# Kernel optimization log

Hardware: AMD Instinct MI355X
Metric: run time of the kernel (lower is better)

Reference implementation:

```python
import jax, jax.numpy as jnp
import numpy as np

B, E, M, H, NH = 256, 16384, 65536, 128, 4
HD = H // NH
LQ, LK = 128, 384  # padded lengths for to_dense_batch (safe upper bounds on group size)


def to_dense_batch(x, batch, num_graphs, max_len):
    # batch is sorted; position within group = global index - group start
    n = x.shape[0]
    start = jnp.searchsorted(batch, jnp.arange(num_graphs))
    pos = jnp.clip(jnp.arange(n) - start[batch], 0, max_len - 1)
    dense = jnp.zeros((num_graphs, max_len, x.shape[-1]), x.dtype).at[batch, pos].set(x)
    mask = jnp.zeros((num_graphs, max_len), bool).at[batch, pos].set(True)
    return dense, mask, pos


def setup_inputs() -> dict:
    key = jax.random.key(0)
    ks = jax.random.split(key, 9)
    edge_attr = jax.random.normal(ks[0], (E, H), jnp.float32)
    edge_index = jax.random.randint(ks[1], (2, E), 0, 4096)
    incoming_edges_list = jax.random.randint(ks[2], (M,), 0, E)
    incoming_edges_batch = jnp.sort(jax.random.randint(ks[3], (M,), 0, B))
    edge_batch = jnp.sort(jax.random.randint(ks[4], (E,), 0, B))
    s = 1.0 / np.sqrt(H)
    s2 = 1.0 / np.sqrt(2 * H)
    in_proj_w = jax.random.uniform(ks[5], (3 * H, H), jnp.float32, -s, s)
    in_proj_b = jnp.zeros((3 * H,), jnp.float32)
    out_proj_w = jax.random.uniform(ks[6], (H, H), jnp.float32, -s, s)
    out_proj_b = jnp.zeros((H,), jnp.float32)
    w1 = jax.random.uniform(ks[7], (2 * H, H), jnp.float32, -s, s)
    b1 = jnp.zeros((2 * H,), jnp.float32)
    w2 = jax.random.uniform(ks[8], (H, 2 * H), jnp.float32, -s2, s2)
    b2 = jnp.zeros((H,), jnp.float32)
    return dict(edge_index=edge_index, edge_attr=edge_attr,
                incoming_edges_list=incoming_edges_list,
                incoming_edges_batch=incoming_edges_batch, edge_batch=edge_batch,
                in_proj_w=in_proj_w, in_proj_b=in_proj_b,
                out_proj_w=out_proj_w, out_proj_b=out_proj_b,
                w1=w1, b1=b1, w2=w2, b2=b2)


def reference(edge_index, edge_attr, incoming_edges_list, incoming_edges_batch,
              edge_batch, in_proj_w, in_proj_b, out_proj_w, out_proj_b,
              w1, b1, w2, b2):
    # pad queries (edges per graph) and keys (gathered incoming messages per graph)
    q_dense, q_mask, q_pos = to_dense_batch(edge_attr, edge_batch, B, LQ)
    gathered = edge_attr[incoming_edges_list]                     # [M, H]
    k_dense, k_mask, _ = to_dense_batch(gathered, incoming_edges_batch, B, LK)

    wq, wk, wv = in_proj_w[:H], in_proj_w[H:2 * H], in_proj_w[2 * H:]
    bq, bk, bv = in_proj_b[:H], in_proj_b[H:2 * H], in_proj_b[2 * H:]
    q = (q_dense @ wq.T + bq).reshape(B, LQ, NH, HD)
    k = (k_dense @ wk.T + bk).reshape(B, LK, NH, HD)
    v = (k_dense @ wv.T + bv).reshape(B, LK, NH, HD)

    logits = jnp.einsum('bqhd,bkhd->bhqk', q, k) / np.sqrt(HD)
    logits = jnp.where(k_mask[:, None, None, :], logits, -1e9)   # key_padding_mask
    attn = jax.nn.softmax(logits, axis=-1)
    ctx = jnp.einsum('bhqk,bkhd->bqhd', attn, v).reshape(B, LQ, H)
    att_dense = ctx @ out_proj_w.T + out_proj_b                   # [B, LQ, H]

    # scatter back to ragged edge order (equiv. to dense[mask] for sorted batch)
    updated = att_dense[edge_batch, q_pos]                        # [E, H]
    att = edge_attr + updated
    ffn = jax.nn.relu(att @ w1.T + b1) @ w2.T + b2
    return att + ffn
```

## Files before the change

### kernel.cpp

```cpp
#include <hip/hip_runtime.h>
#include <hip/hip_bf16.h>

constexpr int B  = 256;
constexpr int E  = 16384;
constexpr int M  = 65536;
constexpr int H  = 128;
constexpr int NH = 4;
constexpr int HD = 32;
constexpr int LQ = 128;
constexpr int LK = 384;

constexpr int WQ_OFF  = 0;
constexpr int WK_OFF  = 16384;
constexpr int WV_OFF  = 32768;
constexpr int OPW_OFF = 49152;
constexpr int W1_OFF  = 65536;
constexpr int W2_OFF  = 98304;
constexpr int W_TOTAL = 131072;

typedef __attribute__((ext_vector_type(8))) short bf16x8;
typedef __attribute__((ext_vector_type(8))) unsigned short u16x8;
typedef __attribute__((ext_vector_type(4))) float f32x4;

__device__ __forceinline__ ushort f2bf(float x) {
  union { float f; unsigned u; } v; v.f = x;
  unsigned r = (v.u + 0x7FFFu + ((v.u >> 16) & 1u)) >> 16;
  return (ushort)r;
}
__device__ __forceinline__ unsigned pack2bf(float a, float b) {
  return (unsigned)f2bf(a) | ((unsigned)f2bf(b) << 16);
}

__global__ __launch_bounds__(256) void k_starts_prep(
    const int* __restrict__ eb, const int* __restrict__ ieb,
    int* __restrict__ sq, int* __restrict__ sk,
    const float* __restrict__ in_proj_w, const float* __restrict__ opw,
    const float* __restrict__ w1, const float* __restrict__ w2,
    ushort* __restrict__ Wb) {
  const int bx = blockIdx.x, t = threadIdx.x;
  if (bx == 0) {
    for (int i = t; i <= B; i += 256) {
      int lo = 0, hi = E;
      while (lo < hi) { int mid = (lo + hi) >> 1; if (eb[mid] < i) lo = mid + 1; else hi = mid; }
      sq[i] = lo;
      lo = 0; hi = M;
      while (lo < hi) { int mid = (lo + hi) >> 1; if (ieb[mid] < i) lo = mid + 1; else hi = mid; }
      sk[i] = lo;
    }
  } else {
    int i = ((bx - 1) * 256 + t) * 4;
    if (i < W_TOTAL) {
      float4 v;
      if (i < OPW_OFF)      v = *(const float4*)(in_proj_w + i);
      else if (i < W1_OFF)  v = *(const float4*)(opw + (i - OPW_OFF));
      else if (i < W2_OFF)  v = *(const float4*)(w1 + (i - W1_OFF));
      else                  v = *(const float4*)(w2 + (i - W2_OFF));
      ushort4 o; o.x = f2bf(v.x); o.y = f2bf(v.y); o.z = f2bf(v.z); o.w = f2bf(v.w);
      *(ushort4*)(Wb + i) = o;
    }
  }
}

__global__ __launch_bounds__(256) void k_proj_all(
    const float* __restrict__ edge_attr, const ushort* __restrict__ Wb,
    const float* __restrict__ in_proj_b,
    ushort* __restrict__ Qall, ushort* __restrict__ Kall, ushort* __restrict__ Vall) {
  constexpr int IP = 136;
  __shared__ ushort inL[32 * IP];
  const int t = threadIdx.x;
  const int row0 = blockIdx.x * 32;
  for (int idx = t; idx < 32 * 32; idx += 256) {
    int r = idx >> 5, c = idx & 31;
    float4 v = ((const float4*)(edge_attr + (size_t)(row0 + r) * H))[c];
    ushort4 o; o.x = f2bf(v.x); o.y = f2bf(v.y); o.z = f2bf(v.z); o.w = f2bf(v.w);
    *(ushort4*)(inL + r * IP + c * 4) = o;
  }
  __syncthreads();
  const int w = t >> 6, lane = t & 63, g = lane >> 4, l15 = lane & 15;
  const int wr = (w & 1) * 16, ch = w >> 1;
  bf16x8 a[4];
#pragma unroll
  for (int kc = 0; kc < 4; kc++)
    a[kc] = *(const bf16x8*)(inL + (wr + l15) * IP + kc * 32 + g * 8);
  const int row = row0 + wr + l15;
#pragma unroll
  for (int p = 0; p < 3; p++) {
    const int woff = WQ_OFF + p * 16384;
    const float* bias = in_proj_b + p * H;
    ushort* dst = (p == 0) ? Qall : (p == 1) ? Kall : Vall;
#pragma unroll
    for (int ci = 0; ci < 4; ci++) {
      int ct = ch * 4 + ci;
      f32x4 acc = {0.f, 0.f, 0.f, 0.f};
#pragma unroll
      for (int kc = 0; kc < 4; kc++) {
        bf16x8 bw = *(const bf16x8*)(Wb + woff + (size_t)(ct * 16 + l15) * H + kc * 32 + g * 8);
        acc = __builtin_amdgcn_mfma_f32_16x16x32_bf16(bw, a[kc], acc, 0, 0, 0);
      }
      int oc = ct * 16 + 4 * g;
      float4 bb = *(const float4*)(bias + oc);
      ushort4 v;
      v.x = f2bf(acc[0] + bb.x); v.y = f2bf(acc[1] + bb.y);
      v.z = f2bf(acc[2] + bb.z); v.w = f2bf(acc[3] + bb.w);
      *(ushort4*)(dst + (size_t)row * H + oc) = v;
    }
  }
}

__global__ __launch_bounds__(256, 4) void k_attn_g(
    const ushort* __restrict__ Qall, const ushort* __restrict__ Kall,
    const ushort* __restrict__ Vall, const int* __restrict__ iel,
    const float* __restrict__ in_proj_b,
    const int* __restrict__ sq, const int* __restrict__ sk,
    ushort* __restrict__ CtxB) {
  constexpr int VP = 388;
  __shared__ ushort VTl[HD * VP];
  __shared__ int srcL[LK];

  const int b = blockIdx.x, h = blockIdx.y;
  const int t = threadIdx.x;
  const int q0 = sq[b], lenq = sq[b + 1] - q0;
  const int k0 = sk[b], lenk = sk[b + 1] - k0;
  const int nq = lenq < LQ ? lenq : LQ;
  const int nk = lenk < LK ? lenk : LK;
  const int nkc = (nk + 63) & ~63;
  const int nqt = (nq + 15) >> 4;

  const int w = t >> 6, lane = t & 63, g = lane >> 4, l15 = lane & 15;
  const int chb = h * HD;

  for (int idx = t; idx < nk; idx += 256) {
    int kj = k0 + idx;
    if (lenk > LK && idx == LK - 1) kj = k0 + lenk - 1;
    srcL[idx] = iel[kj];
  }
  for (int idx = t; idx < nk * 4; idx += 256) {
    int row = idx >> 2, c = idx & 3;
    int kj = k0 + row;
    if (lenk > LK && row == LK - 1) kj = k0 + lenk - 1;
    int src = iel[kj];
    u16x8 v = *(const u16x8*)(Vall + (size_t)src * H + chb + c * 8);
#pragma unroll
    for (int j = 0; j < 8; j++) VTl[(c * 8 + j) * VP + row] = v[j];
  }
  for (int idx = t; idx < ((nkc - nk) << 5); idx += 256) {
    int d = idx & 31, k = nk + (idx >> 5);
    VTl[d * VP + k] = 0;
  }
  __syncthreads();

  const float scale = 0.17677669529663687f;
  for (int qt = w; qt < nqt; qt += 4) {
    int slot = qt * 16 + l15;
    bool valid = slot < nq;
    int src = q0 + slot;
    if (lenq > LQ && slot == LQ - 1) src = q0 + lenq - 1;
    if (!valid) src = q0;
    bf16x8 bq = *(const bf16x8*)(Qall + (size_t)src * H + chb + g * 8);

    f32x4 o0 = {0.f, 0.f, 0.f, 0.f}, o1 = {0.f, 0.f, 0.f, 0.f};
    float m = -3.0e38f, s = 0.f;
    for (int kc = 0; kc < nk; kc += 64) {
      int r0 = kc + l15, r1 = kc + 16 + l15, r2 = kc + 32 + l15, r3 = kc + 48 + l15;
      int s0_ = (r0 < nk) ? srcL[r0] : 0;
      int s1_ = (r1 < nk) ? srcL[r1] : 0;
      int s2_ = (r2 < nk) ? srcL[r2] : 0;
      int s3_ = (r3 < nk) ? srcL[r3] : 0;
      bf16x8 a0 = *(const bf16x8*)(Kall + (size_t)s0_ * H + chb + g * 8);
      bf16x8 a1 = *(const bf16x8*)(Kall + (size_t)s1_ * H + chb + g * 8);
      bf16x8 a2 = *(const bf16x8*)(Kall + (size_t)s2_ * H + chb + g * 8);
      bf16x8 a3 = *(const bf16x8*)(Kall + (size_t)s3_ * H + chb + g * 8);
      f32x4 z = {0.f, 0.f, 0.f, 0.f};
      f32x4 st0 = __builtin_amdgcn_mfma_f32_16x16x32_bf16(a0, bq, z, 0, 0, 0);
      f32x4 st1 = __builtin_amdgcn_mfma_f32_16x16x32_bf16(a1, bq, z, 0, 0, 0);
      f32x4 st2 = __builtin_amdgcn_mfma_f32_16x16x32_bf16(a2, bq, z, 0, 0, 0);
      f32x4 st3 = __builtin_amdgcn_mfma_f32_16x16x32_bf16(a3, bq, z, 0, 0, 0);
      float p[16];
#pragma unroll
      for (int r = 0; r < 4; r++) {
        p[r]      = (kc + 4 * g + r < nk)      ? st0[r] * scale : -1e30f;
        p[4 + r]  = (kc + 16 + 4 * g + r < nk) ? st1[r] * scale : -1e30f;
        p[8 + r]  = (kc + 32 + 4 * g + r < nk) ? st2[r] * scale : -1e30f;
        p[12 + r] = (kc + 48 + 4 * g + r < nk) ? st3[r] * scale : -1e30f;
      }
      float pm = p[0];
#pragma unroll
      for (int r = 1; r < 16; r++) pm = fmaxf(pm, p[r]);
      pm = fmaxf(pm, __shfl_xor(pm, 16));
      pm = fmaxf(pm, __shfl_xor(pm, 32));
      float mn = fmaxf(m, pm);
      float corr = __expf(m - mn);
      float rs = 0.f;
#pragma unroll
      for (int r = 0; r < 16; r++) { p[r] = __expf(p[r] - mn); rs += p[r]; }
      rs += __shfl_xor(rs, 16);
      rs += __shfl_xor(rs, 32);
      s = s * corr + rs;
      m = mn;
      unsigned pkw[4][2];
#pragma unroll
      for (int i = 0; i < 4; i++) {
        pkw[i][0] = pack2bf(p[4 * i + 0], p[4 * i + 1]);
        pkw[i][1] = pack2bf(p[4 * i + 2], p[4 * i + 3]);
      }
      union { int i[4]; bf16x8 v; } pb0, pb1;
#pragma unroll
      for (int j = 0; j < 4; j++) {
        int sl = (2 * (g & 1) + (j >> 1)) * 16 + l15;
        int a_ = __shfl((int)pkw[0][j & 1], sl);
        int b_ = __shfl((int)pkw[1][j & 1], sl);
        int c_ = __shfl((int)pkw[2][j & 1], sl);
        int d_ = __shfl((int)pkw[3][j & 1], sl);
        pb0.i[j] = (g < 2) ? a_ : b_;
        pb1.i[j] = (g < 2) ? c_ : d_;
      }
      bf16x8 av00 = *(const bf16x8*)(VTl + l15 * VP + kc + 8 * g);
      bf16x8 av01 = *(const bf16x8*)(VTl + l15 * VP + kc + 32 + 8 * g);
      bf16x8 av10 = *(const bf16x8*)(VTl + (16 + l15) * VP + kc + 8 * g);
      bf16x8 av11 = *(const bf16x8*)(VTl + (16 + l15) * VP + kc + 32 + 8 * g);
#pragma unroll
      for (int r = 0; r < 4; r++) { o0[r] *= corr; o1[r] *= corr; }
      o0 = __builtin_amdgcn_mfma_f32_16x16x32_bf16(av00, pb0.v, o0, 0, 0, 0);
      o0 = __builtin_amdgcn_mfma_f32_16x16x32_bf16(av01, pb1.v, o0, 0, 0, 0);
      o1 = __builtin_amdgcn_mfma_f32_16x16x32_bf16(av10, pb0.v, o1, 0, 0, 0);
      o1 = __builtin_amdgcn_mfma_f32_16x16x32_bf16(av11, pb1.v, o1, 0, 0, 0);
    }
    if (valid) {
      int qi = q0 + slot;
      if (lenq > LQ && slot == LQ - 1) qi = q0 + lenq - 1;
      ushort* outp = CtxB + (size_t)qi * H + chb;
      if (nk > 0) {
        float inv = 1.f / s;
        ushort4 v0, v1;
#pragma unroll
        for (int r = 0; r < 4; r++) { ((ushort*)&v0)[r] = f2bf(o0[r] * inv); ((ushort*)&v1)[r] = f2bf(o1[r] * inv); }
        *(ushort4*)(outp + 4 * g) = v0;
        *(ushort4*)(outp + 16 + 4 * g) = v1;
      } else {
        const float* bv = in_proj_b + 2 * H + chb;
        ushort4 v0, v1;
#pragma unroll
        for (int r = 0; r < 4; r++) { ((ushort*)&v0)[r] = f2bf(bv[4 * g + r]); ((ushort*)&v1)[r] = f2bf(bv[16 + 4 * g + r]); }
        *(ushort4*)(outp + 4 * g) = v0;
        *(ushort4*)(outp + 16 + 4 * g) = v1;
      }
    }
  }
}

__global__ __launch_bounds__(256) void k_out_ffn_mfma(
    const ushort* __restrict__ CtxB, const float* __restrict__ edge_attr,
    const int* __restrict__ sq, const int* __restrict__ eb,
    const ushort* __restrict__ Wb, const float* __restrict__ opb,
    const float* __restrict__ b1, const float* __restrict__ b2,
    float* __restrict__ out) {
  constexpr int IP = 136;
  constexpr int HP = 264;
  __shared__ ushort attB[16 * IP];
  __shared__ ushort h1L[16 * HP];
  const int t = threadIdx.x;
  const int row0 = blockIdx.x * 16;

  for (int idx = t; idx < 16 * 16; idx += 256) {
    int r = idx >> 4, c = idx & 15;
    int i = row0 + r;
    int bb = eb[i];
    int qq0 = sq[bb];
    int lenq = sq[bb + 1] - qq0;
    int src = i;
    if (lenq > LQ && (i - qq0) >= LQ - 1) src = qq0 + lenq - 1;
    *(u16x8*)(attB + r * IP + c * 8) = *(const u16x8*)(CtxB + (size_t)src * H + c * 8);
  }
  __syncthreads();

  const int w = t >> 6, lane = t & 63, g = lane >> 4, l15 = lane & 15;
  const int row = row0 + l15;
  bf16x8 ca[4];
#pragma unroll
  for (int kc = 0; kc < 4; kc++)
    ca[kc] = *(const bf16x8*)(attB + l15 * IP + kc * 32 + g * 8);
  __syncthreads();

  float att[2][4];
#pragma unroll
  for (int ci = 0; ci < 2; ci++) {
    int ct = w * 2 + ci;
    f32x4 acc = {0.f, 0.f, 0.f, 0.f};
#pragma unroll
    for (int kc = 0; kc < 4; kc++) {
      bf16x8 bw = *(const bf16x8*)(Wb + OPW_OFF + (size_t)(ct * 16 + l15) * H + kc * 32 + g * 8);
      acc = __builtin_amdgcn_mfma_f32_16x16x32_bf16(bw, ca[kc], acc, 0, 0, 0);
    }
    int oc = ct * 16 + 4 * g;
    float4 bo = *(const float4*)(opb + oc);
    float4 ea = *(const float4*)(edge_attr + (size_t)row * H + oc);
    ushort4 v;
    att[ci][0] = acc[0] + bo.x + ea.x; v.x = f2bf(att[ci][0]);
    att[ci][1] = acc[1] + bo.y + ea.y; v.y = f2bf(att[ci][1]);
    att[ci][2] = acc[2] + bo.z + ea.z; v.z = f2bf(att[ci][2]);
    att[ci][3] = acc[3] + bo.w + ea.w; v.w = f2bf(att[ci][3]);
    *(ushort4*)(attB + l15 * IP + oc) = v;
  }
  __syncthreads();

  bf16x8 aa[4];
#pragma unroll
  for (int kc = 0; kc < 4; kc++)
    aa[kc] = *(const bf16x8*)(attB + l15 * IP + kc * 32 + g * 8);
#pragma unroll
  for (int ci = 0; ci < 4; ci++) {
    int ct = w * 4 + ci;
    f32x4 acc = {0.f, 0.f, 0.f, 0.f};
#pragma unroll
    for (int kc = 0; kc < 4; kc++) {
      bf16x8 bw = *(const bf16x8*)(Wb + W1_OFF + (size_t)(ct * 16 + l15) * H + kc * 32 + g * 8);
      acc = __builtin_amdgcn_mfma_f32_16x16x32_bf16(bw, aa[kc], acc, 0, 0, 0);
    }
    int oc = ct * 16 + 4 * g;
    float4 bb = *(const float4*)(b1 + oc);
    ushort4 v;
    v.x = f2bf(fmaxf(acc[0] + bb.x, 0.f)); v.y = f2bf(fmaxf(acc[1] + bb.y, 0.f));
    v.z = f2bf(fmaxf(acc[2] + bb.z, 0.f)); v.w = f2bf(fmaxf(acc[3] + bb.w, 0.f));
    *(ushort4*)(h1L + l15 * HP + oc) = v;
  }
  __syncthreads();

  bf16x8 ha[8];
#pragma unroll
  for (int kc = 0; kc < 8; kc++)
    ha[kc] = *(const bf16x8*)(h1L + l15 * HP + kc * 32 + g * 8);
#pragma unroll
  for (int ci = 0; ci < 2; ci++) {
    int ct = w * 2 + ci;
    f32x4 acc = {0.f, 0.f, 0.f, 0.f};
#pragma unroll
    for (int kc = 0; kc < 8; kc++) {
      bf16x8 bw = *(const bf16x8*)(Wb + W2_OFF + (size_t)(ct * 16 + l15) * 2 * H + kc * 32 + g * 8);
      acc = __builtin_amdgcn_mfma_f32_16x16x32_bf16(bw, ha[kc], acc, 0, 0, 0);
    }
    int oc = ct * 16 + 4 * g;
    float4 bb = *(const float4*)(b2 + oc);
    float4 o;
    o.x = att[ci][0] + acc[0] + bb.x;
    o.y = att[ci][1] + acc[1] + bb.y;
    o.z = att[ci][2] + acc[2] + bb.z;
    o.w = att[ci][3] + acc[3] + bb.w;
    *(float4*)(out + (size_t)row * H + oc) = o;
  }
}

extern "C" void kernel_launch(void* const* d_in, const int* in_sizes, int n_in,
                              void* d_out, int out_size, void* d_ws, size_t ws_size,
                              hipStream_t stream) {
  const float* edge_attr = (const float*)d_in[1];
  const int*   iel       = (const int*)d_in[2];
  const int*   ieb       = (const int*)d_in[3];
  const int*   eb        = (const int*)d_in[4];
  const float* in_proj_w = (const float*)d_in[5];
  const float* in_proj_b = (const float*)d_in[6];
  const float* opw       = (const float*)d_in[7];
  const float* opb       = (const float*)d_in[8];
  const float* w1        = (const float*)d_in[9];
  const float* b1        = (const float*)d_in[10];
  const float* w2        = (const float*)d_in[11];
  const float* b2        = (const float*)d_in[12];
  float* out = (float*)d_out;

  char* ws = (char*)d_ws;
  int* sq = (int*)ws;
  int* sk = (int*)(ws + 2048);
  ushort* CtxB = (ushort*)(ws + 4096);
  ushort* Wb   = CtxB + (size_t)E * H;
  ushort* Qall = Wb + W_TOTAL;
  ushort* Kall = Qall + (size_t)E * H;
  ushort* Vall = Kall + (size_t)E * H;

  k_starts_prep<<<dim3(129), dim3(256), 0, stream>>>(eb, ieb, sq, sk, in_proj_w, opw, w1, w2, Wb);
  k_proj_all<<<dim3(E / 32), dim3(256), 0, stream>>>(edge_attr, Wb, in_proj_b, Qall, Kall, Vall);
  k_attn_g<<<dim3(B, NH), dim3(256), 0, stream>>>(Qall, Kall, Vall, iel, in_proj_b, sq, sk, CtxB);
  k_out_ffn_mfma<<<dim3(E / 16), dim3(256), 0, stream>>>(CtxB, edge_attr, sq, eb, Wb, opb, b1, b2, out);
}
```

Baseline: 83.30 us.

## Drop prep kernel, convert weights inline, and store Q/K/V head-major

Removes the separate prep kernel. Group starts are now found by binary search inside the attention and FFN kernels, and fp32 weights are converted to bf16 on load inside the MFMA loops. Q/K/V are stored head-major ([NH][E][HD]), so each gathered 64-byte row is contiguous per head, and V gathers reuse the shared srcL indices. This saves one launch and its serialization, at the cost of reading fp32 weights twice as wide and repeating the conversion in every block.

```diff
diff --git a/kernel.cpp b/kernel.cpp
--- a/kernel.cpp
+++ b/kernel.cpp
@@ -10,14 +10,6 @@
 constexpr int LQ = 128;
 constexpr int LK = 384;
 
-constexpr int WQ_OFF  = 0;
-constexpr int WK_OFF  = 16384;
-constexpr int WV_OFF  = 32768;
-constexpr int OPW_OFF = 49152;
-constexpr int W1_OFF  = 65536;
-constexpr int W2_OFF  = 98304;
-constexpr int W_TOTAL = 131072;
-
 typedef __attribute__((ext_vector_type(8))) short bf16x8;
 typedef __attribute__((ext_vector_type(8))) unsigned short u16x8;
 typedef __attribute__((ext_vector_type(4))) float f32x4;
@@ -30,41 +22,21 @@
 __device__ __forceinline__ unsigned pack2bf(float a, float b) {
   return (unsigned)f2bf(a) | ((unsigned)f2bf(b) << 16);
 }
-
-__global__ __launch_bounds__(256) void k_starts_prep(
-    const int* __restrict__ eb, const int* __restrict__ ieb,
-    int* __restrict__ sq, int* __restrict__ sk,
-    const float* __restrict__ in_proj_w, const float* __restrict__ opw,
-    const float* __restrict__ w1, const float* __restrict__ w2,
-    ushort* __restrict__ Wb) {
-  const int bx = blockIdx.x, t = threadIdx.x;
-  if (bx == 0) {
-    for (int i = t; i <= B; i += 256) {
-      int lo = 0, hi = E;
-      while (lo < hi) { int mid = (lo + hi) >> 1; if (eb[mid] < i) lo = mid + 1; else hi = mid; }
-      sq[i] = lo;
-      lo = 0; hi = M;
-      while (lo < hi) { int mid = (lo + hi) >> 1; if (ieb[mid] < i) lo = mid + 1; else hi = mid; }
-      sk[i] = lo;
-    }
-  } else {
-    int i = ((bx - 1) * 256 + t) * 4;
-    if (i < W_TOTAL) {
-      float4 v;
-      if (i < OPW_OFF)      v = *(const float4*)(in_proj_w + i);
-      else if (i < W1_OFF)  v = *(const float4*)(opw + (i - OPW_OFF));
-      else if (i < W2_OFF)  v = *(const float4*)(w1 + (i - W1_OFF));
-      else                  v = *(const float4*)(w2 + (i - W2_OFF));
-      ushort4 o; o.x = f2bf(v.x); o.y = f2bf(v.y); o.z = f2bf(v.z); o.w = f2bf(v.w);
-      *(ushort4*)(Wb + i) = o;
-    }
-  }
+__device__ __forceinline__ bf16x8 ldw8(const float* __restrict__ p) {
+  float4 a = *(const float4*)p;
+  float4 b = *(const float4*)(p + 4);
+  union { unsigned u[4]; bf16x8 v; } r;
+  r.u[0] = pack2bf(a.x, a.y);
+  r.u[1] = pack2bf(a.z, a.w);
+  r.u[2] = pack2bf(b.x, b.y);
+  r.u[3] = pack2bf(b.z, b.w);
+  return r.v;
 }
 
 __global__ __launch_bounds__(256) void k_proj_all(
-    const float* __restrict__ edge_attr, const ushort* __restrict__ Wb,
+    const float* __restrict__ edge_attr, const float* __restrict__ in_proj_w,
     const float* __restrict__ in_proj_b,
-    ushort* __restrict__ Qall, ushort* __restrict__ Kall, ushort* __restrict__ Vall) {
+    ushort* __restrict__ Qh, ushort* __restrict__ Kh, ushort* __restrict__ Vh) {
   constexpr int IP = 136;
   __shared__ ushort inL[32 * IP];
   const int t = threadIdx.x;
@@ -85,16 +57,15 @@
   const int row = row0 + wr + l15;
 #pragma unroll
   for (int p = 0; p < 3; p++) {
-    const int woff = WQ_OFF + p * 16384;
     const float* bias = in_proj_b + p * H;
-    ushort* dst = (p == 0) ? Qall : (p == 1) ? Kall : Vall;
+    ushort* dst = (p == 0) ? Qh : (p == 1) ? Kh : Vh;
 #pragma unroll
     for (int ci = 0; ci < 4; ci++) {
       int ct = ch * 4 + ci;
       f32x4 acc = {0.f, 0.f, 0.f, 0.f};
 #pragma unroll
       for (int kc = 0; kc < 4; kc++) {
-        bf16x8 bw = *(const bf16x8*)(Wb + woff + (size_t)(ct * 16 + l15) * H + kc * 32 + g * 8);
+        bf16x8 bw = ldw8(in_proj_w + (size_t)(p * H + ct * 16 + l15) * H + kc * 32 + g * 8);
         acc = __builtin_amdgcn_mfma_f32_16x16x32_bf16(bw, a[kc], acc, 0, 0, 0);
       }
       int oc = ct * 16 + 4 * g;
@@ -102,31 +73,43 @@
       ushort4 v;
       v.x = f2bf(acc[0] + bb.x); v.y = f2bf(acc[1] + bb.y);
       v.z = f2bf(acc[2] + bb.z); v.w = f2bf(acc[3] + bb.w);
-      *(ushort4*)(dst + (size_t)row * H + oc) = v;
+      *(ushort4*)(dst + (size_t)(oc >> 5) * E * HD + (size_t)row * HD + (oc & 31)) = v;
     }
   }
 }
 
 __global__ __launch_bounds__(256, 4) void k_attn_g(
-    const ushort* __restrict__ Qall, const ushort* __restrict__ Kall,
-    const ushort* __restrict__ Vall, const int* __restrict__ iel,
-    const float* __restrict__ in_proj_b,
-    const int* __restrict__ sq, const int* __restrict__ sk,
-    ushort* __restrict__ CtxB) {
+    const ushort* __restrict__ Qh, const ushort* __restrict__ Kh,
+    const ushort* __restrict__ Vh, const int* __restrict__ iel,
+    const int* __restrict__ eb, const int* __restrict__ ieb,
+    const float* __restrict__ in_proj_b, ushort* __restrict__ CtxB) {
   constexpr int VP = 388;
   __shared__ ushort VTl[HD * VP];
   __shared__ int srcL[LK];
+  __shared__ int meta[4];
 
   const int b = blockIdx.x, h = blockIdx.y;
   const int t = threadIdx.x;
-  const int q0 = sq[b], lenq = sq[b + 1] - q0;
-  const int k0 = sk[b], lenk = sk[b + 1] - k0;
+  if (t < 4) {
+    int target = (t & 1) ? b + 1 : b;
+    const int* arr = (t < 2) ? eb : ieb;
+    int n = (t < 2) ? E : M;
+    int lo = 0, hi = n;
+    while (lo < hi) { int mid = (lo + hi) >> 1; if (arr[mid] < target) lo = mid + 1; else hi = mid; }
+    meta[t] = lo;
+  }
+  __syncthreads();
+  const int q0 = meta[0], lenq = meta[1] - meta[0];
+  const int k0 = meta[2], lenk = meta[3] - meta[2];
   const int nq = lenq < LQ ? lenq : LQ;
   const int nk = lenk < LK ? lenk : LK;
   const int nkc = (nk + 63) & ~63;
   const int nqt = (nq + 15) >> 4;
 
   const int w = t >> 6, lane = t & 63, g = lane >> 4, l15 = lane & 15;
+  const ushort* Qhh = Qh + (size_t)h * E * HD;
+  const ushort* Khh = Kh + (size_t)h * E * HD;
+  const ushort* Vhh = Vh + (size_t)h * E * HD;
   const int chb = h * HD;
 
   for (int idx = t; idx < nk; idx += 256) {
@@ -134,12 +117,11 @@
     if (lenk > LK && idx == LK - 1) kj = k0 + lenk - 1;
     srcL[idx] = iel[kj];
   }
+  __syncthreads();
   for (int idx = t; idx < nk * 4; idx += 256) {
     int row = idx >> 2, c = idx & 3;
-    int kj = k0 + row;
-    if (lenk > LK && row == LK - 1) kj = k0 + lenk - 1;
-    int src = iel[kj];
-    u16x8 v = *(const u16x8*)(Vall + (size_t)src * H + chb + c * 8);
+    int src = srcL[row];
+    u16x8 v = *(const u16x8*)(Vhh + (size_t)src * HD + c * 8);
 #pragma unroll
     for (int j = 0; j < 8; j++) VTl[(c * 8 + j) * VP + row] = v[j];
   }
@@ -156,7 +138,7 @@
     int src = q0 + slot;
     if (lenq > LQ && slot == LQ - 1) src = q0 + lenq - 1;
     if (!valid) src = q0;
-    bf16x8 bq = *(const bf16x8*)(Qall + (size_t)src * H + chb + g * 8);
+    bf16x8 bq = *(const bf16x8*)(Qhh + (size_t)src * HD + g * 8);
 
     f32x4 o0 = {0.f, 0.f, 0.f, 0.f}, o1 = {0.f, 0.f, 0.f, 0.f};
     float m = -3.0e38f, s = 0.f;
@@ -166,10 +148,10 @@
       int s1_ = (r1 < nk) ? srcL[r1] : 0;
       int s2_ = (r2 < nk) ? srcL[r2] : 0;
       int s3_ = (r3 < nk) ? srcL[r3] : 0;
-      bf16x8 a0 = *(const bf16x8*)(Kall + (size_t)s0_ * H + chb + g * 8);
-      bf16x8 a1 = *(const bf16x8*)(Kall + (size_t)s1_ * H + chb + g * 8);
-      bf16x8 a2 = *(const bf16x8*)(Kall + (size_t)s2_ * H + chb + g * 8);
-      bf16x8 a3 = *(const bf16x8*)(Kall + (size_t)s3_ * H + chb + g * 8);
+      bf16x8 a0 = *(const bf16x8*)(Khh + (size_t)s0_ * HD + g * 8);
+      bf16x8 a1 = *(const bf16x8*)(Khh + (size_t)s1_ * HD + g * 8);
+      bf16x8 a2 = *(const bf16x8*)(Khh + (size_t)s2_ * HD + g * 8);
+      bf16x8 a3 = *(const bf16x8*)(Khh + (size_t)s3_ * HD + g * 8);
       f32x4 z = {0.f, 0.f, 0.f, 0.f};
       f32x4 st0 = __builtin_amdgcn_mfma_f32_16x16x32_bf16(a0, bq, z, 0, 0, 0);
       f32x4 st1 = __builtin_amdgcn_mfma_f32_16x16x32_bf16(a1, bq, z, 0, 0, 0);
@@ -250,26 +232,37 @@
 
 __global__ __launch_bounds__(256) void k_out_ffn_mfma(
     const ushort* __restrict__ CtxB, const float* __restrict__ edge_attr,
-    const int* __restrict__ sq, const int* __restrict__ eb,
-    const ushort* __restrict__ Wb, const float* __restrict__ opb,
-    const float* __restrict__ b1, const float* __restrict__ b2,
+    const int* __restrict__ eb,
+    const float* __restrict__ opw, const float* __restrict__ opb,
+    const float* __restrict__ w1, const float* __restrict__ b1,
+    const float* __restrict__ w2, const float* __restrict__ b2,
     float* __restrict__ out) {
   constexpr int IP = 136;
   constexpr int HP = 264;
   __shared__ ushort attB[16 * IP];
   __shared__ ushort h1L[16 * HP];
+  __shared__ int srcRow[16];
   const int t = threadIdx.x;
   const int row0 = blockIdx.x * 16;
 
+  if (t < 16) {
+    int i = row0 + t;
+    int bb = eb[i];
+    int lo = 0, hi = E;
+    while (lo < hi) { int mid = (lo + hi) >> 1; if (eb[mid] < bb) lo = mid + 1; else hi = mid; }
+    int qq0 = lo;
+    hi = E;
+    while (lo < hi) { int mid = (lo + hi) >> 1; if (eb[mid] < bb + 1) lo = mid + 1; else hi = mid; }
+    int lenq = lo - qq0;
+    int src = i;
+    if (lenq > LQ && (i - qq0) >= LQ - 1) src = qq0 + lenq - 1;
+    srcRow[t] = src;
+  }
+  __syncthreads();
+
   for (int idx = t; idx < 16 * 16; idx += 256) {
     int r = idx >> 4, c = idx & 15;
-    int i = row0 + r;
-    int bb = eb[i];
-    int qq0 = sq[bb];
-    int lenq = sq[bb + 1] - qq0;
-    int src = i;
-    if (lenq > LQ && (i - qq0) >= LQ - 1) src = qq0 + lenq - 1;
-    *(u16x8*)(attB + r * IP + c * 8) = *(const u16x8*)(CtxB + (size_t)src * H + c * 8);
+    *(u16x8*)(attB + r * IP + c * 8) = *(const u16x8*)(CtxB + (size_t)srcRow[r] * H + c * 8);
   }
   __syncthreads();
 
@@ -288,7 +281,7 @@
     f32x4 acc = {0.f, 0.f, 0.f, 0.f};
 #pragma unroll
     for (int kc = 0; kc < 4; kc++) {
-      bf16x8 bw = *(const bf16x8*)(Wb + OPW_OFF + (size_t)(ct * 16 + l15) * H + kc * 32 + g * 8);
+      bf16x8 bw = ldw8(opw + (size_t)(ct * 16 + l15) * H + kc * 32 + g * 8);
       acc = __builtin_amdgcn_mfma_f32_16x16x32_bf16(bw, ca[kc], acc, 0, 0, 0);
     }
     int oc = ct * 16 + 4 * g;
@@ -313,7 +306,7 @@
     f32x4 acc = {0.f, 0.f, 0.f, 0.f};
 #pragma unroll
     for (int kc = 0; kc < 4; kc++) {
-      bf16x8 bw = *(const bf16x8*)(Wb + W1_OFF + (size_t)(ct * 16 + l15) * H + kc * 32 + g * 8);
+      bf16x8 bw = ldw8(w1 + (size_t)(ct * 16 + l15) * H + kc * 32 + g * 8);
       acc = __builtin_amdgcn_mfma_f32_16x16x32_bf16(bw, aa[kc], acc, 0, 0, 0);
     }
     int oc = ct * 16 + 4 * g;
@@ -335,7 +328,7 @@
     f32x4 acc = {0.f, 0.f, 0.f, 0.f};
 #pragma unroll
     for (int kc = 0; kc < 8; kc++) {
-      bf16x8 bw = *(const bf16x8*)(Wb + W2_OFF + (size_t)(ct * 16 + l15) * 2 * H + kc * 32 + g * 8);
+      bf16x8 bw = ldw8(w2 + (size_t)(ct * 16 + l15) * 2 * H + kc * 32 + g * 8);
       acc = __builtin_amdgcn_mfma_f32_16x16x32_bf16(bw, ha[kc], acc, 0, 0, 0);
     }
     int oc = ct * 16 + 4 * g;
@@ -367,16 +360,12 @@
   float* out = (float*)d_out;
 
   char* ws = (char*)d_ws;
-  int* sq = (int*)ws;
-  int* sk = (int*)(ws + 2048);
-  ushort* CtxB = (ushort*)(ws + 4096);
-  ushort* Wb   = CtxB + (size_t)E * H;
-  ushort* Qall = Wb + W_TOTAL;
-  ushort* Kall = Qall + (size_t)E * H;
-  ushort* Vall = Kall + (size_t)E * H;
-
-  k_starts_prep<<<dim3(129), dim3(256), 0, stream>>>(eb, ieb, sq, sk, in_proj_w, opw, w1, w2, Wb);
-  k_proj_all<<<dim3(E / 32), dim3(256), 0, stream>>>(edge_attr, Wb, in_proj_b, Qall, Kall, Vall);
-  k_attn_g<<<dim3(B, NH), dim3(256), 0, stream>>>(Qall, Kall, Vall, iel, in_proj_b, sq, sk, CtxB);
-  k_out_ffn_mfma<<<dim3(E / 16), dim3(256), 0, stream>>>(CtxB, edge_attr, sq, eb, Wb, opb, b1, b2, out);
-}
+  ushort* CtxB = (ushort*)ws;
+  ushort* Qh   = CtxB + (size_t)E * H;
+  ushort* Kh   = Qh + (size_t)E * H;
+  ushort* Vh   = Kh + (size_t)E * H;
+
+  k_proj_all<<<dim3(E / 32), dim3(256), 0, stream>>>(edge_attr, in_proj_w, in_proj_b, Qh, Kh, Vh);
+  k_attn_g<<<dim3(B, NH), dim3(256), 0, stream>>>(Qh, Kh, Vh, iel, eb, ieb, in_proj_b, CtxB);
+  k_out_ffn_mfma<<<dim3(E / 16), dim3(256), 0, stream>>>(CtxB, edge_attr, eb, opw, opb, w1, b1, w2, b2, out);
+}
```

Result: slower. 104.0 us (+24.9%).
